# Kernel optimization log

Hardware: AMD Instinct MI355X
Metric: run time of the kernel (lower is better)

The kernel has to match this reference:

```python
import jax, jax.numpy as jnp
import numpy as np

NUM_HEADS = 16
NEG_INF = jnp.float32(-1e30)


def setup_inputs() -> dict:
    key = jax.random.key(0)
    ks = jax.random.split(key, 6)
    B, S, D = 2, 2048, 1024
    s = 1.0 / np.sqrt(D)
    return {
        "x": jax.random.normal(ks[0], (B, S, D), dtype=jnp.float32),
        "attention_mask": jnp.ones((B, S), dtype=jnp.int32),
        "Wq": jax.random.normal(ks[1], (D, D), dtype=jnp.float32) * s,
        "bq": jnp.zeros((D,), dtype=jnp.float32),
        "Wk": jax.random.normal(ks[2], (D, D), dtype=jnp.float32) * s,
        "bk": jnp.zeros((D,), dtype=jnp.float32),
        "Wv": jax.random.normal(ks[3], (D, D), dtype=jnp.float32) * s,
        "bv": jnp.zeros((D,), dtype=jnp.float32),
        "Wo": jax.random.normal(ks[4], (D, D), dtype=jnp.float32) * s,
        "bo": jnp.zeros((D,), dtype=jnp.float32),
    }


def reference(x, attention_mask, Wq, bq, Wk, bk, Wv, bv, Wo, bo):
    B, S, D = x.shape
    H = NUM_HEADS
    hd = D // H
    scale = jnp.float32(1.0 / np.sqrt(hd))

    def split_heads(t):  # (B,S,D) -> (B,H,S,hd)
        return t.reshape(B, S, H, hd).transpose(0, 2, 1, 3)

    Q = split_heads(x @ Wq + bq)
    K = split_heads(x @ Wk + bk)
    V = split_heads(x @ Wv + bv)

    scores = jnp.einsum("bhqd,bhkd->bhqk", Q, K) * scale  # (B,H,S,S)

    # causal mask: disallow k > q
    causal = jnp.triu(jnp.ones((S, S), dtype=bool), k=1)
    scores = jnp.where(causal[None, None, :, :], NEG_INF, scores)

    # padding mask over keys: (B,1,1,S); 1=valid, 0=pad
    valid = attention_mask[:, None, None, :] > 0
    scores = jnp.where(valid, scores, NEG_INF)

    attn = jax.nn.softmax(scores, axis=-1)  # dropout is identity in eval
    ctx = jnp.einsum("bhqk,bhkd->bhqd", attn, V)
    ctx = ctx.transpose(0, 2, 1, 3).reshape(B, S, D)
    return ctx @ Wo + bo
```

## Files before the change

### kernel.cpp

```cpp
#include <hip/hip_runtime.h>
#include <hip/hip_bf16.h>


using bf16 = __hip_bfloat16;
typedef __attribute__((ext_vector_type(8))) short bf16x8_t;
typedef __attribute__((ext_vector_type(4))) float f32x4_t;

#define MFMA(a, b, c) __builtin_amdgcn_mfma_f32_16x16x32_bf16((a), (b), (c), 0, 0, 0)

constexpr int SEQ = 2048;
constexpr int DIM = 1024;
constexpr int HD  = 64;
constexpr int MROWS = 2 * SEQ;

__device__ __forceinline__ void gload_lds16(const bf16* g, bf16* l) {
    __builtin_amdgcn_global_load_lds(
        (const __attribute__((address_space(1))) unsigned int*)g,
        (__attribute__((address_space(3))) unsigned int*)l, 16, 0, 0);
}

__device__ __forceinline__ ushort4 pack4(f32x4_t v) {
    ushort4 u;
    u.x = __builtin_bit_cast(unsigned short, __float2bfloat16(v[0]));
    u.y = __builtin_bit_cast(unsigned short, __float2bfloat16(v[1]));
    u.z = __builtin_bit_cast(unsigned short, __float2bfloat16(v[2]));
    u.w = __builtin_bit_cast(unsigned short, __float2bfloat16(v[3]));
    return u;
}

__global__ __launch_bounds__(256) void k_convert_x(const float4* __restrict__ x,
                                                   ushort4* __restrict__ xb) {
    int i = blockIdx.x * 256 + threadIdx.x;
    float4 v = x[i];
    ushort4 o;
    o.x = __builtin_bit_cast(unsigned short, __float2bfloat16(v.x));
    o.y = __builtin_bit_cast(unsigned short, __float2bfloat16(v.y));
    o.z = __builtin_bit_cast(unsigned short, __float2bfloat16(v.z));
    o.w = __builtin_bit_cast(unsigned short, __float2bfloat16(v.w));
    xb[i] = o;
}

__global__ __launch_bounds__(256) void k_transpose_w(const float* __restrict__ W0,
                                                     const float* __restrict__ W1,
                                                     const float* __restrict__ W2,
                                                     const float* __restrict__ W3,
                                                     bf16* __restrict__ Wt) {
    const float* W = blockIdx.z == 0 ? W0 : blockIdx.z == 1 ? W1
                   : blockIdx.z == 2 ? W2 : W3;
    bf16* out = Wt + (size_t)blockIdx.z * DIM * DIM;
    __shared__ float tile[64][65];
    int r0 = blockIdx.x * 64, c0 = blockIdx.y * 64;
    int t = threadIdx.x;
    int c = t & 63, rq = t >> 6;
#pragma unroll
    for (int j = 0; j < 16; ++j) {
        int r = rq + j * 4;
        tile[r][c] = W[(size_t)(r0 + r) * DIM + c0 + c];
    }
    __syncthreads();
#pragma unroll
    for (int j = 0; j < 16; ++j) {
        int n = rq + j * 4;
        out[(size_t)(c0 + n) * DIM + r0 + c] = __float2bfloat16(tile[c][n]);
    }
}

__global__ __launch_bounds__(256) void k_gemm_qkv(const bf16* __restrict__ A,
                                                  const bf16* __restrict__ Bt,
                                                  const float* __restrict__ bq,
                                                  const float* __restrict__ bk,
                                                  const float* __restrict__ bv,
                                                  bf16* __restrict__ Out) {
    constexpr int K = DIM;
    __shared__ bf16 As[128 * 32];
    __shared__ bf16 Bs[128 * 32];
    int t = threadIdx.x;
    int l = t & 63;
    int w = t >> 6;
    int lr = l & 15, lg = l >> 4;
    int wr = w >> 1, wc = w & 1;
    int m0 = blockIdx.x * 128;
    int n0 = blockIdx.y * 128;

    f32x4_t acc[4][4] = {};

    int sr = t >> 2;
    int sc = (t & 3) * 8;
    const bf16* ga = A + (size_t)(m0 + sr) * K + sc;
    const bf16* gb = Bt + (size_t)(n0 + sr) * K + sc;
    bf16* wa = As + t * 8;
    bf16* wb = Bs + t * 8;

    for (int k0 = 0; k0 < K; k0 += 32) {
        gload_lds16(ga, wa);
        gload_lds16(ga + (size_t)64 * K, wa + 2048);
        gload_lds16(gb, wb);
        gload_lds16(gb + (size_t)64 * K, wb + 2048);
        ga += 32; gb += 32;
        __syncthreads();
        bf16x8_t af[4], bfv[4];
#pragma unroll
        for (int mi = 0; mi < 4; ++mi)
            af[mi] = *(const bf16x8_t*)&As[(wr * 64 + mi * 16 + lr) * 32 + lg * 8];
#pragma unroll
        for (int ni = 0; ni < 4; ++ni)
            bfv[ni] = *(const bf16x8_t*)&Bs[(wc * 64 + ni * 16 + lr) * 32 + lg * 8];
#pragma unroll
        for (int mi = 0; mi < 4; ++mi)
#pragma unroll
            for (int ni = 0; ni < 4; ++ni)
                acc[mi][ni] = MFMA(af[mi], bfv[ni], acc[mi][ni]);
        __syncthreads();
    }

    int seg = n0 >> 10;
    int nl = (n0 & 1023) + wc * 64;
    const float* bias = seg == 0 ? bq : seg == 1 ? bk : bv;
    float alpha = seg == 0 ? 0.125f : 1.0f;
    bf16* outp = Out + (size_t)seg * MROWS * DIM;
#pragma unroll
    for (int mi = 0; mi < 4; ++mi) {
#pragma unroll
        for (int ni = 0; ni < 4; ++ni) {
            int row = m0 + wr * 64 + mi * 16 + lg * 4;
            int col = nl + ni * 16 + lr;
            float bb = bias[col];
#pragma unroll
            for (int r = 0; r < 4; ++r) {
                float v = (acc[mi][ni][r] + bb) * alpha;
                outp[(size_t)(row + r) * DIM + col] = __float2bfloat16(v);
            }
        }
    }
}

__global__ __launch_bounds__(256) void k_transpose_v(const bf16* __restrict__ Vb,
                                                     bf16* __restrict__ Vt) {
    int s0 = blockIdx.x * 64;
    int bh = blockIdx.y;
    int b = bh >> 4, h = bh & 15;
    __shared__ bf16 tile[64][66];
    int t = threadIdx.x;
    int c = t & 63, rq = t >> 6;
#pragma unroll
    for (int j = 0; j < 16; ++j) {
        int s = rq + j * 4;
        tile[s][c] = Vb[(size_t)(b * SEQ + s0 + s) * DIM + h * HD + c];
    }
    __syncthreads();
#pragma unroll
    for (int j = 0; j < 16; ++j) {
        int d = rq + j * 4;
        Vt[((size_t)bh * HD + d) * SEQ + s0 + c] = tile[c][d];
    }
}

__global__ __launch_bounds__(256) void k_attn(const bf16* __restrict__ Qb,
                                              const bf16* __restrict__ Kb,
                                              const bf16* __restrict__ Vt,
                                              const int* __restrict__ amask,
                                              bf16* __restrict__ Ctx) {
    int qt = 15 - blockIdx.x;
    int bh = blockIdx.y;
    int b = bh >> 4, h = bh & 15;
    int t = threadIdx.x;
    int w = t >> 6, l = t & 63;
    int lr = l & 15, lg = l >> 4;
    int m0 = qt * 128 + w * 32;

    __shared__ bf16  Kl[2][64 * 64];
    __shared__ bf16  Vl[2][64 * 64];
    __shared__ float Bl[SEQ];
    __shared__ bf16  Ps[4][16 * 72];

    const bf16* vtb   = Vt + (size_t)bh * HD * SEQ;
    const bf16* kbase = Kb + (size_t)b * SEQ * DIM + h * HD;

    auto stage = [&](int kt, int bufi) {
#pragma unroll
        for (int c = 0; c < 2; ++c) {
            int P = t * 16 + c * 4096;
            int row = P >> 7;
            int Lb = (P & 127) ^ ((row & 7) << 4);
            gload_lds16(kbase + (size_t)(kt * 64 + row) * DIM + (Lb >> 1),
                        (bf16*)((char*)&Kl[bufi][0] + P));
        }
#pragma unroll
        for (int c = 0; c < 2; ++c) {
            int P = t * 16 + c * 4096;
            int row = P >> 7;
            int Lb = (P & 127) ^ ((row & 7) << 4);
            gload_lds16(vtb + (size_t)row * SEQ + kt * 64 + (Lb >> 1),
                        (bf16*)((char*)&Vl[bufi][0] + P));
        }
    };

    int nkt = 2 * qt + 2;
    stage(0, 0);

#pragma unroll
    for (int j = 0; j < 2; ++j) {
        int4 a4 = ((const int4*)(amask + b * SEQ))[t * 2 + j];
        int i = (t * 2 + j) * 4;
        Bl[i + 0] = a4.x > 0 ? 0.f : -1e30f;
        Bl[i + 1] = a4.y > 0 ? 0.f : -1e30f;
        Bl[i + 2] = a4.z > 0 ? 0.f : -1e30f;
        Bl[i + 3] = a4.w > 0 ? 0.f : -1e30f;
    }

    const bf16* qbase = Qb + (size_t)(b * SEQ + m0 + lr) * DIM + h * HD;
    bf16x8_t qf[2][2];
#pragma unroll
    for (int qi = 0; qi < 2; ++qi)
#pragma unroll
        for (int ks = 0; ks < 2; ++ks)
            qf[qi][ks] = *(const bf16x8_t*)(qbase + (size_t)qi * 16 * DIM + ks * 32 + lg * 8);

    f32x4_t o[2][4] = {};
    float mrow[2] = {-1e30f, -1e30f}, lrow[2] = {0.f, 0.f};
    bf16* ps = &Ps[w][0];

    __syncthreads();
    int buf = 0;
    for (int kt = 0; kt < nkt; ++kt) {
        if (kt + 1 < nkt) stage(kt + 1, buf ^ 1);
        const char* Klb = (const char*)&Kl[buf][0];
        const char* Vlb = (const char*)&Vl[buf][0];

        bf16x8_t kf[4][2];
#pragma unroll
        for (int ni = 0; ni < 4; ++ni) {
            int row = ni * 16 + lr;
#pragma unroll
            for (int ks = 0; ks < 2; ++ks)
                kf[ni][ks] = *(const bf16x8_t*)(Klb + row * 128 +
                                 ((ks * 64 + lg * 16) ^ ((row & 7) << 4)));
        }
        bf16x8_t vf[4][2];
#pragma unroll
        for (int ni = 0; ni < 4; ++ni) {
            int row = ni * 16 + lr;
#pragma unroll
            for (int kc = 0; kc < 2; ++kc)
                vf[ni][kc] = *(const bf16x8_t*)(Vlb + row * 128 +
                                 ((kc * 64 + lg * 16) ^ ((row & 7) << 4)));
        }
        f32x4_t b4[4];
#pragma unroll
        for (int ni = 0; ni < 4; ++ni)
            b4[ni] = *(const f32x4_t*)&Bl[kt * 64 + ni * 16 + lg * 4];

#pragma unroll
        for (int qi = 0; qi < 2; ++qi) {
            f32x4_t s[4];
#pragma unroll
            for (int ni = 0; ni < 4; ++ni) {
                f32x4_t a = {0.f, 0.f, 0.f, 0.f};
                a = MFMA(kf[ni][0], qf[qi][0], a);
                a = MFMA(kf[ni][1], qf[qi][1], a);
                s[ni] = a + b4[ni];
            }
            int q = m0 + qi * 16 + lr;
            if (kt * 64 + 63 > m0 + qi * 16) {
#pragma unroll
                for (int ni = 0; ni < 4; ++ni)
#pragma unroll
                    for (int r = 0; r < 4; ++r) {
                        int key = kt * 64 + ni * 16 + lg * 4 + r;
                        if (key > q) s[ni][r] = -1e30f;
                    }
            }
            float tm = fmaxf(fmaxf(fmaxf(s[0][0], s[0][1]), fmaxf(s[0][2], s[0][3])),
                             fmaxf(fmaxf(s[1][0], s[1][1]), fmaxf(s[1][2], s[1][3])));
            float tm2 = fmaxf(fmaxf(fmaxf(s[2][0], s[2][1]), fmaxf(s[2][2], s[2][3])),
                              fmaxf(fmaxf(s[3][0], s[3][1]), fmaxf(s[3][2], s[3][3])));
            tm = fmaxf(tm, tm2);
            tm = fmaxf(tm, __shfl_xor(tm, 16));
            tm = fmaxf(tm, __shfl_xor(tm, 32));
            float mnew = fmaxf(mrow[qi], tm);
            float al = __expf(mrow[qi] - mnew);
            mrow[qi] = mnew;
            float rs = 0.f;
#pragma unroll
            for (int ni = 0; ni < 4; ++ni) {
#pragma unroll
                for (int r = 0; r < 4; ++r) {
                    float p = __expf(s[ni][r] - mnew);
                    s[ni][r] = p;
                    rs += p;
                }
            }
            rs += __shfl_xor(rs, 16);
            rs += __shfl_xor(rs, 32);
            lrow[qi] = lrow[qi] * al + rs;
#pragma unroll
            for (int ni = 0; ni < 4; ++ni)
                o[qi][ni] *= al;
            asm volatile("" ::: "memory");
#pragma unroll
            for (int ni = 0; ni < 4; ++ni)
                *(ushort4*)&ps[lr * 72 + ni * 16 + lg * 4] = pack4(s[ni]);
            asm volatile("s_waitcnt lgkmcnt(0)" ::: "memory");
            __builtin_amdgcn_sched_barrier(0);
            bf16x8_t pf[2];
#pragma unroll
            for (int kc = 0; kc < 2; ++kc)
                pf[kc] = *(const bf16x8_t*)&ps[lr * 72 + kc * 32 + lg * 8];
#pragma unroll
            for (int ni = 0; ni < 4; ++ni) {
                o[qi][ni] = MFMA(vf[ni][0], pf[0], o[qi][ni]);
                o[qi][ni] = MFMA(vf[ni][1], pf[1], o[qi][ni]);
            }
        }
        __syncthreads();
        buf ^= 1;
    }

#pragma unroll
    for (int qi = 0; qi < 2; ++qi) {
        float inv = 1.0f / lrow[qi];
        size_t row = (size_t)(b * SEQ + m0 + qi * 16 + lr);
#pragma unroll
        for (int ni = 0; ni < 4; ++ni) {
            f32x4_t v = o[qi][ni];
            v *= inv;
            *(ushort4*)&Ctx[row * DIM + h * HD + ni * 16 + lg * 4] = pack4(v);
        }
    }
}

__global__ __launch_bounds__(256) void k_gemm_out(const bf16* __restrict__ A,
                                                  const bf16* __restrict__ Bt,
                                                  const float* __restrict__ bias,
                                                  float* __restrict__ Out) {
    constexpr int K = DIM;
    __shared__ bf16 As[128 * 32];
    __shared__ bf16 Bs[128 * 32];
    int t = threadIdx.x;
    int l = t & 63;
    int w = t >> 6;
    int lr = l & 15, lg = l >> 4;
    int wr = w >> 1, wc = w & 1;
    int m0 = blockIdx.x * 128;
    int n0 = blockIdx.y * 128;

    f32x4_t acc[4][4] = {};

    int sr = t >> 2;
    int sc = (t & 3) * 8;
    const bf16* ga = A + (size_t)(m0 + sr) * K + sc;
    const bf16* gb = Bt + (size_t)(n0 + sr) * K + sc;
    bf16* wa = As + t * 8;
    bf16* wb = Bs + t * 8;

    for (int k0 = 0; k0 < K; k0 += 32) {
        gload_lds16(ga, wa);
        gload_lds16(ga + (size_t)64 * K, wa + 2048);
        gload_lds16(gb, wb);
        gload_lds16(gb + (size_t)64 * K, wb + 2048);
        ga += 32; gb += 32;
        __syncthreads();
        bf16x8_t af[4], bfv[4];
#pragma unroll
        for (int mi = 0; mi < 4; ++mi)
            af[mi] = *(const bf16x8_t*)&As[(wr * 64 + mi * 16 + lr) * 32 + lg * 8];
#pragma unroll
        for (int ni = 0; ni < 4; ++ni)
            bfv[ni] = *(const bf16x8_t*)&Bs[(wc * 64 + ni * 16 + lr) * 32 + lg * 8];
#pragma unroll
        for (int mi = 0; mi < 4; ++mi)
#pragma unroll
            for (int ni = 0; ni < 4; ++ni)
                acc[mi][ni] = MFMA(af[mi], bfv[ni], acc[mi][ni]);
        __syncthreads();
    }

    int nl = n0 + wc * 64;
#pragma unroll
    for (int mi = 0; mi < 4; ++mi) {
#pragma unroll
        for (int ni = 0; ni < 4; ++ni) {
            int row = m0 + wr * 64 + mi * 16 + lg * 4;
            int col = nl + ni * 16 + lr;
            float bb = bias[col];
#pragma unroll
            for (int r = 0; r < 4; ++r)
                Out[(size_t)(row + r) * DIM + col] = acc[mi][ni][r] + bb;
        }
    }
}

extern "C" void kernel_launch(void* const* d_in, const int* in_sizes, int n_in,
                              void* d_out, int out_size, void* d_ws, size_t ws_size,
                              hipStream_t stream) {
    const float* x  = (const float*)d_in[0];
    const int*   am = (const int*)d_in[1];
    const float* Wq = (const float*)d_in[2];
    const float* bq = (const float*)d_in[3];
    const float* Wk = (const float*)d_in[4];
    const float* bk = (const float*)d_in[5];
    const float* Wv = (const float*)d_in[6];
    const float* bv = (const float*)d_in[7];
    const float* Wo = (const float*)d_in[8];
    const float* bo = (const float*)d_in[9];

    char* ws = (char*)d_ws;
    const size_t MB = (size_t)1 << 20;
    bf16* xb  = (bf16*)(ws + 0 * MB);
    bf16* Wt  = (bf16*)(ws + 8 * MB);
    bf16* Qb  = (bf16*)(ws + 16 * MB);
    bf16* Vb  = (bf16*)(ws + 32 * MB);
    bf16* Vt  = (bf16*)(ws + 40 * MB);
    bf16* Ctx = (bf16*)(ws + 48 * MB);

    k_convert_x<<<dim3(MROWS * DIM / 4 / 256), 256, 0, stream>>>(
        (const float4*)x, (ushort4*)xb);
    k_transpose_w<<<dim3(16, 16, 4), 256, 0, stream>>>(Wq, Wk, Wv, Wo, Wt);
    k_gemm_qkv<<<dim3(32, 24), 256, 0, stream>>>(xb, Wt, bq, bk, bv, Qb);
    k_transpose_v<<<dim3(32, 32), 256, 0, stream>>>(Vb, Vt);
    k_attn<<<dim3(16, 32), 256, 0, stream>>>(Qb, Qb + (size_t)MROWS * DIM, Vt, am, Ctx);
    k_gemm_out<<<dim3(32, 8), 256, 0, stream>>>(Ctx, Wt + (size_t)3 * DIM * DIM, bo,
                                                (float*)d_out);
}
```

Before: 233.3 us.

## Batch both QK tiles before softmax, use exp2 with folded scale, and reorder blocks

The Q scale now carries a log2(e) factor so the softmax can call the hardware exp2 directly instead of __expf. The attention loop runs the score MFMAs for both query sub-tiles first, then does softmax for both, then issues both PV MFMA groups after a single LDS wait. MFMA phases get raised wave priority, which is meant to let waves overlap math with the softmax work of other waves. The grid is flattened and blocks are ordered in a serpentine way over causal tile sizes to balance load across CUs. The cost is a larger P buffer in LDS and more live registers.

```diff
diff --git a/kernel.cpp b/kernel.cpp
--- a/kernel.cpp
+++ b/kernel.cpp
@@ -26,6 +26,14 @@
     u.z = __builtin_bit_cast(unsigned short, __float2bfloat16(v[2]));
     u.w = __builtin_bit_cast(unsigned short, __float2bfloat16(v[3]));
     return u;
+}
+
+__device__ __forceinline__ float fexp2(float x) {
+#if __has_builtin(__builtin_amdgcn_exp2f)
+    return __builtin_amdgcn_exp2f(x);
+#else
+    return exp2f(x);
+#endif
 }
 
 __global__ __launch_bounds__(256) void k_convert_x(const float4* __restrict__ x,
@@ -116,7 +124,7 @@
     int seg = n0 >> 10;
     int nl = (n0 & 1023) + wc * 64;
     const float* bias = seg == 0 ? bq : seg == 1 ? bk : bv;
-    float alpha = seg == 0 ? 0.125f : 1.0f;
+    float alpha = seg == 0 ? 0.18033688011112042f : 1.0f;
     bf16* outp = Out + (size_t)seg * MROWS * DIM;
 #pragma unroll
     for (int mi = 0; mi < 4; ++mi) {
@@ -160,8 +168,10 @@
                                               const bf16* __restrict__ Vt,
                                               const int* __restrict__ amask,
                                               bf16* __restrict__ Ctx) {
-    int qt = 15 - blockIdx.x;
-    int bh = blockIdx.y;
+    int i = blockIdx.x;
+    int rank = (i < 256) ? i : 767 - i;
+    int qt = 15 - (rank >> 5);
+    int bh = rank & 31;
     int b = bh >> 4, h = bh & 15;
     int t = threadIdx.x;
     int w = t >> 6, l = t & 63;
@@ -171,7 +181,7 @@
     __shared__ bf16  Kl[2][64 * 64];
     __shared__ bf16  Vl[2][64 * 64];
     __shared__ float Bl[SEQ];
-    __shared__ bf16  Ps[4][16 * 72];
+    __shared__ bf16  Ps[4][16 * 136];
 
     const bf16* vtb   = Vt + (size_t)bh * HD * SEQ;
     const bf16* kbase = Kb + (size_t)b * SEQ * DIM + h * HD;
@@ -201,11 +211,11 @@
 #pragma unroll
     for (int j = 0; j < 2; ++j) {
         int4 a4 = ((const int4*)(amask + b * SEQ))[t * 2 + j];
-        int i = (t * 2 + j) * 4;
-        Bl[i + 0] = a4.x > 0 ? 0.f : -1e30f;
-        Bl[i + 1] = a4.y > 0 ? 0.f : -1e30f;
-        Bl[i + 2] = a4.z > 0 ? 0.f : -1e30f;
-        Bl[i + 3] = a4.w > 0 ? 0.f : -1e30f;
+        int idx = (t * 2 + j) * 4;
+        Bl[idx + 0] = a4.x > 0 ? 0.f : -1e30f;
+        Bl[idx + 1] = a4.y > 0 ? 0.f : -1e30f;
+        Bl[idx + 2] = a4.z > 0 ? 0.f : -1e30f;
+        Bl[idx + 3] = a4.w > 0 ? 0.f : -1e30f;
     }
 
     const bf16* qbase = Qb + (size_t)(b * SEQ + m0 + lr) * DIM + h * HD;
@@ -250,16 +260,22 @@
         for (int ni = 0; ni < 4; ++ni)
             b4[ni] = *(const f32x4_t*)&Bl[kt * 64 + ni * 16 + lg * 4];
 
-#pragma unroll
-        for (int qi = 0; qi < 2; ++qi) {
-            f32x4_t s[4];
+        f32x4_t s[2][4];
+        __builtin_amdgcn_s_setprio(1);
+#pragma unroll
+        for (int qi = 0; qi < 2; ++qi)
 #pragma unroll
             for (int ni = 0; ni < 4; ++ni) {
                 f32x4_t a = {0.f, 0.f, 0.f, 0.f};
                 a = MFMA(kf[ni][0], qf[qi][0], a);
                 a = MFMA(kf[ni][1], qf[qi][1], a);
-                s[ni] = a + b4[ni];
+                s[qi][ni] = a + b4[ni];
             }
+        __builtin_amdgcn_s_setprio(0);
+
+        asm volatile("" ::: "memory");
+#pragma unroll
+        for (int qi = 0; qi < 2; ++qi) {
             int q = m0 + qi * 16 + lr;
             if (kt * 64 + 63 > m0 + qi * 16) {
 #pragma unroll
@@ -267,26 +283,26 @@
 #pragma unroll
                     for (int r = 0; r < 4; ++r) {
                         int key = kt * 64 + ni * 16 + lg * 4 + r;
-                        if (key > q) s[ni][r] = -1e30f;
+                        if (key > q) s[qi][ni][r] = -1e30f;
                     }
             }
-            float tm = fmaxf(fmaxf(fmaxf(s[0][0], s[0][1]), fmaxf(s[0][2], s[0][3])),
-                             fmaxf(fmaxf(s[1][0], s[1][1]), fmaxf(s[1][2], s[1][3])));
-            float tm2 = fmaxf(fmaxf(fmaxf(s[2][0], s[2][1]), fmaxf(s[2][2], s[2][3])),
-                              fmaxf(fmaxf(s[3][0], s[3][1]), fmaxf(s[3][2], s[3][3])));
-            tm = fmaxf(tm, tm2);
+            float tm = fmaxf(
+                fmaxf(fmaxf(fmaxf(s[qi][0][0], s[qi][0][1]), fmaxf(s[qi][0][2], s[qi][0][3])),
+                      fmaxf(fmaxf(s[qi][1][0], s[qi][1][1]), fmaxf(s[qi][1][2], s[qi][1][3]))),
+                fmaxf(fmaxf(fmaxf(s[qi][2][0], s[qi][2][1]), fmaxf(s[qi][2][2], s[qi][2][3])),
+                      fmaxf(fmaxf(s[qi][3][0], s[qi][3][1]), fmaxf(s[qi][3][2], s[qi][3][3]))));
             tm = fmaxf(tm, __shfl_xor(tm, 16));
             tm = fmaxf(tm, __shfl_xor(tm, 32));
             float mnew = fmaxf(mrow[qi], tm);
-            float al = __expf(mrow[qi] - mnew);
+            float al = fexp2(mrow[qi] - mnew);
             mrow[qi] = mnew;
             float rs = 0.f;
 #pragma unroll
             for (int ni = 0; ni < 4; ++ni) {
 #pragma unroll
                 for (int r = 0; r < 4; ++r) {
-                    float p = __expf(s[ni][r] - mnew);
-                    s[ni][r] = p;
+                    float p = fexp2(s[qi][ni][r] - mnew);
+                    s[qi][ni][r] = p;
                     rs += p;
                 }
             }
@@ -296,22 +312,27 @@
 #pragma unroll
             for (int ni = 0; ni < 4; ++ni)
                 o[qi][ni] *= al;
-            asm volatile("" ::: "memory");
 #pragma unroll
             for (int ni = 0; ni < 4; ++ni)
-                *(ushort4*)&ps[lr * 72 + ni * 16 + lg * 4] = pack4(s[ni]);
-            asm volatile("s_waitcnt lgkmcnt(0)" ::: "memory");
-            __builtin_amdgcn_sched_barrier(0);
+                *(ushort4*)&ps[lr * 136 + qi * 64 + ni * 16 + lg * 4] = pack4(s[qi][ni]);
+        }
+        asm volatile("s_waitcnt lgkmcnt(0)" ::: "memory");
+        __builtin_amdgcn_sched_barrier(0);
+
+        __builtin_amdgcn_s_setprio(1);
+#pragma unroll
+        for (int qi = 0; qi < 2; ++qi) {
             bf16x8_t pf[2];
 #pragma unroll
             for (int kc = 0; kc < 2; ++kc)
-                pf[kc] = *(const bf16x8_t*)&ps[lr * 72 + kc * 32 + lg * 8];
+                pf[kc] = *(const bf16x8_t*)&ps[lr * 136 + qi * 64 + kc * 32 + lg * 8];
 #pragma unroll
             for (int ni = 0; ni < 4; ++ni) {
                 o[qi][ni] = MFMA(vf[ni][0], pf[0], o[qi][ni]);
                 o[qi][ni] = MFMA(vf[ni][1], pf[1], o[qi][ni]);
             }
         }
+        __builtin_amdgcn_s_setprio(0);
         __syncthreads();
         buf ^= 1;
     }
@@ -418,7 +439,7 @@
     k_transpose_w<<<dim3(16, 16, 4), 256, 0, stream>>>(Wq, Wk, Wv, Wo, Wt);
     k_gemm_qkv<<<dim3(32, 24), 256, 0, stream>>>(xb, Wt, bq, bk, bv, Qb);
     k_transpose_v<<<dim3(32, 32), 256, 0, stream>>>(Vb, Vt);
-    k_attn<<<dim3(16, 32), 256, 0, stream>>>(Qb, Qb + (size_t)MROWS * DIM, Vt, am, Ctx);
+    k_attn<<<dim3(512), 256, 0, stream>>>(Qb, Qb + (size_t)MROWS * DIM, Vt, am, Ctx);
     k_gemm_out<<<dim3(32, 8), 256, 0, stream>>>(Ctx, Wt + (size_t)3 * DIM * DIM, bo,
                                                 (float*)d_out);
 }
```

New measurement: 216.4 us. 7.3% less time.
